# Optimization experiments

Hardware: AMD Instinct MI355X
Metric: run time of the kernel (lower is better)

The kernel has to match this reference:

```python
import jax, jax.numpy as jnp
import numpy as np

NUM_CLASSES = 26
IGNORE_LABEL = 0
EPSILON = 1e-05


def setup_inputs() -> dict:
    key = jax.random.key(0)
    k1, k2 = jax.random.split(key)
    shape = (2, 192, 192, 192)
    fixed = jax.random.randint(k1, shape, 0, NUM_CLASSES, dtype=jnp.int32)
    moving = jax.random.randint(k2, shape, 0, NUM_CLASSES, dtype=jnp.int32)
    return {"fixed_label_map": fixed, "warped_moving_label_map": moving}


def reference(fixed_label_map, warped_moving_label_map):
    # Equivalent math to: one_hot both maps, elementwise multiply, sum over
    # (batch, D, H, W) per class. one_hot(f)*one_hot(m) is the indicator
    # (f == m == c), so per-class counts via bincount give identical sums
    # without materializing the (N, C, D, H, W) one-hot tensors.
    f = fixed_label_map.reshape(-1)
    m = warped_moving_label_map.reshape(-1)

    fixed_volume = jnp.bincount(f, length=NUM_CLASSES).astype(jnp.float32)
    moving_volume = jnp.bincount(m, length=NUM_CLASSES).astype(jnp.float32)
    # Route mismatched voxels to a dummy bin (index NUM_CLASSES), then drop it.
    match_labels = jnp.where(f == m, f, NUM_CLASSES)
    intersection = jnp.bincount(match_labels, length=NUM_CLASSES + 1)[:NUM_CLASSES].astype(jnp.float32)

    dice = (2.0 * intersection + EPSILON) / (fixed_volume + moving_volume + EPSILON)
    # Drop ignore_label == 0 (valid classes are 1..25).
    dice_valid = dice[1:]
    return 1.0 - dice_valid.mean()
```

## Files before the change

kernel.cpp:

```cpp
#include <hip/hip_runtime.h>

#define NUM_CLASSES 26
#define SUBS 4
#define NCOUNT (3 * NUM_CLASSES)
#define LDSN (NCOUNT * SUBS)
#define NREP 16
#define REPSTRIDE 80
#define GC_WORDS (NREP * REPSTRIDE)
#define TPB 256

__global__ void sdl_zero(unsigned int* __restrict__ c) {
    for (int i = threadIdx.x; i < GC_WORDS; i += TPB) c[i] = 0u;
}

#define HIDX(hist, cls) ((((hist) * NUM_CLASSES) + (cls)) * SUBS + sub)
#define PROC_PAIR(aa, bb)                                                   \
    do {                                                                    \
        atomicAdd(&h[HIDX(0, (aa).x)], 1u);                                 \
        atomicAdd(&h[HIDX(0, (aa).y)], 1u);                                 \
        atomicAdd(&h[HIDX(0, (aa).z)], 1u);                                 \
        atomicAdd(&h[HIDX(0, (aa).w)], 1u);                                 \
        atomicAdd(&h[HIDX(1, (bb).x)], 1u);                                 \
        atomicAdd(&h[HIDX(1, (bb).y)], 1u);                                 \
        atomicAdd(&h[HIDX(1, (bb).z)], 1u);                                 \
        atomicAdd(&h[HIDX(1, (bb).w)], 1u);                                 \
        if ((aa).x == (bb).x) atomicAdd(&h[HIDX(2, (aa).x)], 1u);           \
        if ((aa).y == (bb).y) atomicAdd(&h[HIDX(2, (aa).y)], 1u);           \
        if ((aa).z == (bb).z) atomicAdd(&h[HIDX(2, (aa).z)], 1u);           \
        if ((aa).w == (bb).w) atomicAdd(&h[HIDX(2, (aa).w)], 1u);           \
    } while (0)

__global__ __launch_bounds__(TPB, 2) void sdl_hist(
    const int4* __restrict__ f4, const int4* __restrict__ m4,
    unsigned int* __restrict__ gc, int n4, int nfull) {
    __shared__ unsigned int h[LDSN];
    for (int i = threadIdx.x; i < LDSN; i += TPB) h[i] = 0u;
    __syncthreads();

    const int tid      = blockIdx.x * TPB + threadIdx.x;
    const int nthreads = gridDim.x * TPB;
    const int sub      = threadIdx.x & (SUBS - 1);

    for (int base = tid; base < nfull; base += nthreads * 8) {
        int4 a[8], b[8];
        #pragma unroll
        for (int k = 0; k < 8; ++k) a[k] = f4[base + k * nthreads];
        #pragma unroll
        for (int k = 0; k < 8; ++k) b[k] = m4[base + k * nthreads];
        #pragma unroll
        for (int k = 0; k < 8; ++k) {
            int4 aa = a[k], bb = b[k];
            PROC_PAIR(aa, bb);
        }
    }
    for (int i = nfull + tid; i < n4; i += nthreads) {
        int4 aa = f4[i], bb = m4[i];
        PROC_PAIR(aa, bb);
    }

    __syncthreads();
    unsigned int* rep = gc + (blockIdx.x & (NREP - 1)) * REPSTRIDE;
    for (int i = threadIdx.x; i < NCOUNT; i += TPB) {
        unsigned int v = 0;
        #pragma unroll
        for (int s2 = 0; s2 < SUBS; ++s2) v += h[i * SUBS + s2];
        if (v) atomicAdd(&rep[i], v);
    }
}

__global__ void sdl_finalize(const unsigned int* __restrict__ gc,
                             float* __restrict__ out) {
    __shared__ float vals[NCOUNT];
    if (threadIdx.x < NCOUNT) {
        unsigned int v = 0;
        for (int r = 0; r < NREP; ++r) v += gc[r * REPSTRIDE + threadIdx.x];
        vals[threadIdx.x] = (float)v;
    }
    __syncthreads();
    if (threadIdx.x == 0) {
        const float eps = 1e-5f;
        float s = 0.f;
        for (int c = 1; c < NUM_CLASSES; ++c) {
            float F = vals[c];
            float M = vals[NUM_CLASSES + c];
            float I = vals[2 * NUM_CLASSES + c];
            s += (2.f * I + eps) / (F + M + eps);
        }
        out[0] = 1.f - s / (float)(NUM_CLASSES - 1);
    }
}

extern "C" void kernel_launch(void* const* d_in, const int* in_sizes, int n_in,
                              void* d_out, int out_size, void* d_ws, size_t ws_size,
                              hipStream_t stream) {
    const int* f = (const int*)d_in[0];
    const int* m = (const int*)d_in[1];
    unsigned int* gc = (unsigned int*)d_ws;
    float* out = (float*)d_out;

    int n  = in_sizes[0];
    int n4 = n / 4;

    sdl_zero<<<1, TPB, 0, stream>>>(gc);

    int blocks = n4 / (TPB * 8);
    if (blocks < 1) blocks = 1;
    if (blocks > 4096) blocks = 4096;
    int nthreads = blocks * TPB;
    int nfull = (n4 / (nthreads * 8)) * (nthreads * 8);

    sdl_hist<<<blocks, TPB, 0, stream>>>((const int4*)f, (const int4*)m, gc, n4, nfull);

    sdl_finalize<<<1, 128, 0, stream>>>(gc, out);
}
```

Before: 31.56 us.

## Replace three per-class histograms with a joint 26x26 confusion histogram

Each voxel pair now does one LDS atomic into a joint (fixed, moving) bin instead of two unconditional atomics plus a conditional intersection atomic. Fixed and moving volumes come from row and column sums of the joint histogram, and the intersection comes from its diagonal, all computed in the per-block epilogue. Sub-histogram replication drops from 4 to 2 copies, which may increase same-address atomic contention, and the epilogue does more LDS reads per block.

```diff
diff --git a/kernel.cpp b/kernel.cpp
--- a/kernel.cpp
+++ b/kernel.cpp
@@ -1,9 +1,10 @@
 #include <hip/hip_runtime.h>
 
 #define NUM_CLASSES 26
-#define SUBS 4
+#define NBINS (NUM_CLASSES * NUM_CLASSES)
+#define SUBS 2
+#define LDSN (SUBS * NBINS)
 #define NCOUNT (3 * NUM_CLASSES)
-#define LDSN (NCOUNT * SUBS)
 #define NREP 16
 #define REPSTRIDE 80
 #define GC_WORDS (NREP * REPSTRIDE)
@@ -13,21 +14,12 @@
     for (int i = threadIdx.x; i < GC_WORDS; i += TPB) c[i] = 0u;
 }
 
-#define HIDX(hist, cls) ((((hist) * NUM_CLASSES) + (cls)) * SUBS + sub)
-#define PROC_PAIR(aa, bb)                                                   \
-    do {                                                                    \
-        atomicAdd(&h[HIDX(0, (aa).x)], 1u);                                 \
-        atomicAdd(&h[HIDX(0, (aa).y)], 1u);                                 \
-        atomicAdd(&h[HIDX(0, (aa).z)], 1u);                                 \
-        atomicAdd(&h[HIDX(0, (aa).w)], 1u);                                 \
-        atomicAdd(&h[HIDX(1, (bb).x)], 1u);                                 \
-        atomicAdd(&h[HIDX(1, (bb).y)], 1u);                                 \
-        atomicAdd(&h[HIDX(1, (bb).z)], 1u);                                 \
-        atomicAdd(&h[HIDX(1, (bb).w)], 1u);                                 \
-        if ((aa).x == (bb).x) atomicAdd(&h[HIDX(2, (aa).x)], 1u);           \
-        if ((aa).y == (bb).y) atomicAdd(&h[HIDX(2, (aa).y)], 1u);           \
-        if ((aa).z == (bb).z) atomicAdd(&h[HIDX(2, (aa).z)], 1u);           \
-        if ((aa).w == (bb).w) atomicAdd(&h[HIDX(2, (aa).w)], 1u);           \
+#define PROC_PAIR(aa, bb)                                                    \
+    do {                                                                     \
+        atomicAdd(&h[hb + ((aa).x * NUM_CLASSES + (bb).x)], 1u);             \
+        atomicAdd(&h[hb + ((aa).y * NUM_CLASSES + (bb).y)], 1u);             \
+        atomicAdd(&h[hb + ((aa).z * NUM_CLASSES + (bb).z)], 1u);             \
+        atomicAdd(&h[hb + ((aa).w * NUM_CLASSES + (bb).w)], 1u);             \
     } while (0)
 
 __global__ __launch_bounds__(TPB, 2) void sdl_hist(
@@ -39,7 +31,7 @@
 
     const int tid      = blockIdx.x * TPB + threadIdx.x;
     const int nthreads = gridDim.x * TPB;
-    const int sub      = threadIdx.x & (SUBS - 1);
+    const int hb       = (threadIdx.x & (SUBS - 1)) * NBINS;
 
     for (int base = tid; base < nfull; base += nthreads * 8) {
         int4 a[8], b[8];
@@ -59,12 +51,26 @@
     }
 
     __syncthreads();
+
     unsigned int* rep = gc + (blockIdx.x & (NREP - 1)) * REPSTRIDE;
-    for (int i = threadIdx.x; i < NCOUNT; i += TPB) {
+    const int t = threadIdx.x;
+    if (t < NUM_CLASSES) {
         unsigned int v = 0;
         #pragma unroll
-        for (int s2 = 0; s2 < SUBS; ++s2) v += h[i * SUBS + s2];
-        if (v) atomicAdd(&rep[i], v);
+        for (int j = 0; j < NUM_CLASSES; ++j)
+            v += h[t * NUM_CLASSES + j] + h[NBINS + t * NUM_CLASSES + j];
+        if (v) atomicAdd(&rep[t], v);
+    } else if (t >= 64 && t < 64 + NUM_CLASSES) {
+        int c = t - 64;
+        unsigned int v = 0;
+        #pragma unroll
+        for (int j = 0; j < NUM_CLASSES; ++j)
+            v += h[j * NUM_CLASSES + c] + h[NBINS + j * NUM_CLASSES + c];
+        if (v) atomicAdd(&rep[NUM_CLASSES + c], v);
+    } else if (t >= 128 && t < 128 + NUM_CLASSES) {
+        int c = t - 128;
+        unsigned int v = h[c * NUM_CLASSES + c] + h[NBINS + c * NUM_CLASSES + c];
+        if (v) atomicAdd(&rep[2 * NUM_CLASSES + c], v);
     }
 }
 
```

After: 30.67 us. 2.8% less time.
